# Optimization experiments

Hardware: AMD Instinct MI355X
Metric: run time of the kernel (lower is better)

The kernel has to match this reference:

```python
import jax, jax.numpy as jnp
import numpy as np

D = 1024       # embedding_dim
H = 4096       # mlp_dim
E = 64         # num_experts
K = 3          # top-k
B, S = 2, 2048
C = 512


def setup_inputs() -> dict:
    key = jax.random.key(0)
    ks = jax.random.split(key, 6)
    s = 0.02
    return {
        "x": jax.random.normal(ks[0], (B, S, D), jnp.float32),
        "gate_w": jax.random.normal(ks[1], (D, E), jnp.float32) * s,
        "gate_b": jnp.zeros((E,), jnp.float32),
        "w1": jax.random.normal(ks[2], (E, D, H), jnp.float32) * s,
        "b1": jnp.zeros((E, H), jnp.float32),
        "w2": jax.random.normal(ks[3], (E, H, D), jnp.float32) * s,
        "b2": jnp.zeros((E, D), jnp.float32),
    }


def reference(x, gate_w, gate_b, w1, b1, w2, b2):
    xf = x.reshape(-1, D)                       # [T, D] flattened tokens
    T = xf.shape[0]
    # --- top-k gating (eval mode: clean logits, no noise) ---
    logits = xf @ gate_w + gate_b               # [T, E]
    top_l, top_i = jax.lax.top_k(logits, K)     # [T, K]
    gates = jax.nn.softmax(top_l, axis=-1)      # softmax over the k selected logits
    # --- token permutation / dispatch (capacity-based, order-preserving) ---
    fe = top_i.reshape(-1)                      # [T*K] expert id per assignment
    fg = gates.reshape(-1)                      # [T*K] gate per assignment
    tok = jnp.repeat(jnp.arange(T), K)          # [T*K] source token id
    oh = jax.nn.one_hot(fe, E, dtype=jnp.int32) # [T*K, E]
    pos = (jnp.cumsum(oh, axis=0) * oh).sum(-1) - 1  # slot within expert buffer
    valid = pos < C                             # capacity mask (C sized so nothing drops in practice)
    # scatter tokens into per-expert buffers; OOB (pos>=C) rows dropped
    buf = jnp.zeros((E, C, D), x.dtype).at[fe, pos].set(xf[tok], mode='drop')
    # --- grouped expert MLP: Linear -> exact GELU -> Linear ---
    h = jax.nn.gelu(jnp.einsum('ecd,edh->ech', buf, w1) + b1[:, None, :], approximate=False)
    y = jnp.einsum('ech,ehd->ecd', h, w2) + b2[:, None, :]  # [E, C, D]
    # --- gather back, gate, scatter-add combine ---
    rows = y[fe, jnp.minimum(pos, C - 1)] * (fg * valid.astype(x.dtype))[:, None]
    out = jnp.zeros_like(xf).at[tok].add(rows)
    return out.reshape(x.shape)
```

## Files before the change

kernel.cpp:

```cpp
#include <hip/hip_runtime.h>

#define TTOK 4096
#define DDIM 1024
#define HDIM 4096
#define NEXP 64
#define CAP  512
#define NASN (TTOK*3)

typedef unsigned short u16;
typedef __attribute__((ext_vector_type(8))) short s16x8;
typedef __attribute__((ext_vector_type(4))) short s16x4;
typedef __attribute__((ext_vector_type(4))) float f32x4;

__device__ __forceinline__ u16 f2bf(float f) {
  union { float f; unsigned u; } v; v.f = f;
  unsigned u = v.u;
  return (u16)((u + 0x7fffu + ((u >> 16) & 1u)) >> 16);
}

__device__ __forceinline__ void gl_lds16(const void* g, void* l) {
  __builtin_amdgcn_global_load_lds(
      (const __attribute__((address_space(1))) void*)g,
      (__attribute__((address_space(3))) void*)l, 16, 0, 0);
}

__global__ __launch_bounds__(256) void zero_out(float4* __restrict__ p, int n4) {
  int i = blockIdx.x * 256 + threadIdx.x;
  int st = gridDim.x * 256;
  for (; i < n4; i += st) p[i] = (float4){0.f, 0.f, 0.f, 0.f};
}

__global__ __launch_bounds__(512) void gate_topk(
    const float* __restrict__ x, const float* __restrict__ gw,
    const float* __restrict__ gb, int* __restrict__ fe, float* __restrict__ fg)
{
  int lane = threadIdx.x & 63;
  int wid  = threadIdx.x >> 6;
  int t = blockIdx.x * 8 + wid;
  const float* xr = x + (size_t)t * DDIM;
  float acc = gb[lane];
  #pragma unroll 4
  for (int d = 0; d < DDIM; d++) acc += xr[d] * gw[d * NEXP + lane];

  float v = acc;
  float bv[3]; int bi[3];
  #pragma unroll
  for (int j = 0; j < 3; j++) {
    float mv = v; int mi = lane;
    #pragma unroll
    for (int off = 32; off; off >>= 1) {
      float ov = __shfl_xor(mv, off);
      int   oi = __shfl_xor(mi, off);
      if (ov > mv || (ov == mv && oi < mi)) { mv = ov; mi = oi; }
    }
    bv[j] = mv; bi[j] = mi;
    if (lane == mi) v = -3.4e38f;
  }
  if (lane == 0) {
    float e1 = expf(bv[1] - bv[0]), e2 = expf(bv[2] - bv[0]);
    float inv = 1.0f / (1.0f + e1 + e2);
    fe[t*3+0] = bi[0]; fe[t*3+1] = bi[1]; fe[t*3+2] = bi[2];
    fg[t*3+0] = inv;   fg[t*3+1] = e1*inv; fg[t*3+2] = e2*inv;
  }
}

__global__ __launch_bounds__(64) void scan_pos(
    const int* __restrict__ fe, int* __restrict__ posA,
    int* __restrict__ s2a, int* __restrict__ cnt)
{
  int e = blockIdx.x, lane = threadIdx.x;
  int base = 0;
  for (int i0 = 0; i0 < NASN; i0 += 64) {
    int i = i0 + lane;
    bool m = (fe[i] == e);
    unsigned long long bal = __ballot(m);
    int below = __popcll(bal & ((1ull << lane) - 1ull));
    if (m) {
      int p = base + below;
      posA[i] = p;
      if (p < CAP) s2a[e * CAP + p] = i;
    }
    base += __popcll(bal);
  }
  if (lane == 0) cnt[e] = base < CAP ? base : CAP;
}

__global__ __launch_bounds__(64) void dispatch(
    const float* __restrict__ x, const int* __restrict__ fe,
    const int* __restrict__ posA, u16* __restrict__ bufA)
{
  int a = blockIdx.x;
  int p = posA[a];
  if (p >= CAP) return;
  int e = fe[a];
  int tok = a / 3;
  int l = threadIdx.x;
  const float4* xr = (const float4*)(x + (size_t)tok * DDIM);
  u16* dst = bufA + ((size_t)e * CAP + p) * DDIM;
  #pragma unroll
  for (int j = 0; j < 4; j++) {
    float4 v = xr[j * 64 + l];
    uint2 u;
    u.x = (unsigned)f2bf(v.x) | ((unsigned)f2bf(v.y) << 16);
    u.y = (unsigned)f2bf(v.z) | ((unsigned)f2bf(v.w) << 16);
    *(uint2*)(dst + (size_t)(j * 64 + l) * 4) = u;
  }
}

template<int KTOT, int NTOT, int EPI>
__global__ __launch_bounds__(256, 2) void moe_gemm(
    const u16* __restrict__ Abuf, const float* __restrict__ W,
    const float* __restrict__ bias, u16* __restrict__ hout,
    float* __restrict__ out, const int* __restrict__ cnt,
    const int* __restrict__ s2a, const float* __restrict__ fg, int g0)
{
  constexpr int NCT = NTOT / 128;
  constexpr int NT  = KTOT / 64;
  int NB = gridDim.x;
  int b = blockIdx.x;
  int L = (b & 7) * (NB >> 3) + (b >> 3);
  int tcol = L % NCT;
  int rt   = (L / NCT) & 1;
  int el   = L / (NCT * 2);
  int e    = g0 + el;
  int cnte = cnt[e];
  int c0   = rt * 256;
  if (c0 >= cnte) return;
  int n0 = tcol * 128;

  int tid = threadIdx.x, l = tid & 63, w = tid >> 6;

  __shared__ char AsB[256 * 128];
  __shared__ char BsB[128 * 136];

  const u16* Arows = Abuf + ((size_t)((EPI == 1 ? e : el)) * CAP + c0) * (size_t)KTOT;
  const float* We = W + (size_t)e * KTOT * NTOT;

  int bn = tid & 127, bkg = tid >> 7;
  const float* Wt = We + (size_t)(bkg * 32) * NTOT + n0 + bn;
  char* BsW = BsB + bn * 136 + bkg * 64;

  float brB[32];
  #define LOADB(t) { \
    const float* p_ = Wt + (size_t)(t) * 64 * NTOT; \
    _Pragma("unroll") \
    for (int j_ = 0; j_ < 8; j_++) { \
      _Pragma("unroll") \
      for (int r_ = 0; r_ < 4; r_++) \
        brB[j_ * 4 + r_] = p_[(size_t)(j_ * 4 + r_) * NTOT]; \
    } }
  #define STOREB() { \
    _Pragma("unroll") \
    for (int j_ = 0; j_ < 8; j_++) { \
      uint2 u_; \
      u_.x = (unsigned)f2bf(brB[j_*4+0]) | ((unsigned)f2bf(brB[j_*4+1]) << 16); \
      u_.y = (unsigned)f2bf(brB[j_*4+2]) | ((unsigned)f2bf(brB[j_*4+3]) << 16); \
      *(uint2*)(BsW + j_ * 8) = u_; \
    } }

  f32x4 acc[4][8];
  #pragma unroll
  for (int m = 0; m < 4; m++)
    #pragma unroll
    for (int nn = 0; nn < 8; nn++)
      acc[m][nn] = (f32x4){0.f, 0.f, 0.f, 0.f};

  LOADB(0);

  for (int t = 0; t < NT; ++t) {
    #pragma unroll
    for (int i = 0; i < 8; i++) {
      int r = i * 32 + w * 8 + (l >> 3);
      int cswz = (l & 7) ^ (r & 7);
      const char* gsrc = (const char*)(Arows + (size_t)r * KTOT + (size_t)t * 64) + cswz * 16;
      gl_lds16(gsrc, AsB + (i * 32 + w * 8) * 128);
    }
    STOREB();
    __builtin_amdgcn_sched_barrier(0);
    if (t + 1 < NT) {
      LOADB(t + 1);
      __builtin_amdgcn_sched_barrier(0);
      asm volatile("s_waitcnt vmcnt(32)" ::: "memory");
    } else {
      asm volatile("s_waitcnt vmcnt(0)" ::: "memory");
    }
    asm volatile("s_waitcnt lgkmcnt(0)" ::: "memory");
    __builtin_amdgcn_sched_barrier(0);
    __builtin_amdgcn_s_barrier();
    __builtin_amdgcn_sched_barrier(0);

    #pragma unroll
    for (int k2 = 0; k2 < 2; k2++) {
      int kb = k2 * 32;
      s16x8 af[4], bf8[8];
      #pragma unroll
      for (int m = 0; m < 4; m++) {
        int R = w * 64 + m * 16 + (l & 15);
        int chunk = (kb >> 3) + (l >> 4);
        int sc = chunk ^ (R & 7);
        af[m] = *(const s16x8*)(AsB + R * 128 + sc * 16);
      }
      #pragma unroll
      for (int nn = 0; nn < 8; nn++) {
        int Nn = nn * 16 + (l & 15);
        int kk = kb + (l >> 4) * 8;
        const char* bp = BsB + Nn * 136 + kk * 2;
        union { s16x8 v8; s16x4 v4[2]; } bu;
        bu.v4[0] = *(const s16x4*)bp;
        bu.v4[1] = *(const s16x4*)(bp + 8);
        bf8[nn] = bu.v8;
      }
      #pragma unroll
      for (int m = 0; m < 4; m++)
        #pragma unroll
        for (int nn = 0; nn < 8; nn++)
          acc[m][nn] = __builtin_amdgcn_mfma_f32_16x16x32_bf16(af[m], bf8[nn], acc[m][nn], 0, 0, 0);
    }
    __builtin_amdgcn_s_barrier();
    __builtin_amdgcn_sched_barrier(0);
  }

  int lr = l >> 4, lc = l & 15;
  float bv[8];
  #pragma unroll
  for (int nn = 0; nn < 8; nn++) bv[nn] = bias[(size_t)e * NTOT + n0 + nn * 16 + lc];

  if (EPI == 1) {
    #pragma unroll
    for (int m = 0; m < 4; m++)
      #pragma unroll
      for (int q = 0; q < 4; q++) {
        int rowL = w * 64 + m * 16 + lr * 4 + q;
        if (c0 + rowL < cnte) {
          #pragma unroll
          for (int nn = 0; nn < 8; nn++) {
            float vv = acc[m][nn][q] + bv[nn];
            vv = 0.5f * vv * (1.0f + erff(vv * 0.70710678118f));
            hout[(size_t)(el * CAP + c0 + rowL) * NTOT + (n0 + nn * 16 + lc)] = f2bf(vv);
          }
        }
      }
  } else {
    #pragma unroll
    for (int m = 0; m < 4; m++) {
      int rowbase = w * 64 + m * 16 + lr * 4;
      #pragma unroll
      for (int q = 0; q < 4; q++) {
        int slot = c0 + rowbase + q;
        if (slot < cnte) {
          int aidx = s2a[e * CAP + slot];
          int tok = aidx / 3;
          float gg = fg[aidx];
          #pragma unroll
          for (int nn = 0; nn < 8; nn++) {
            float vv = (acc[m][nn][q] + bv[nn]) * gg;
            atomicAdd(out + (size_t)tok * DDIM + (n0 + nn * 16 + lc), vv);
          }
        }
      }
    }
  }
}

extern "C" void kernel_launch(void* const* d_in, const int* in_sizes, int n_in,
                              void* d_out, int out_size, void* d_ws, size_t ws_size,
                              hipStream_t stream) {
  (void)in_sizes; (void)n_in; (void)ws_size;
  const float* x  = (const float*)d_in[0];
  const float* gw = (const float*)d_in[1];
  const float* gb = (const float*)d_in[2];
  const float* w1 = (const float*)d_in[3];
  const float* b1 = (const float*)d_in[4];
  const float* w2 = (const float*)d_in[5];
  const float* b2 = (const float*)d_in[6];
  float* out = (float*)d_out;

  char* ws = (char*)d_ws;
  int*   fe   = (int*)(ws);
  float* fg   = (float*)(ws + 49152);
  int*   posA = (int*)(ws + 98304);
  int*   s2a  = (int*)(ws + 147456);
  int*   cnt  = (int*)(ws + 278528);
  u16*   bufA = (u16*)(ws + (1 << 20));
  u16*   hbuf = (u16*)(ws + (1 << 20) + 67108864ull);

  zero_out<<<1024, 256, 0, stream>>>((float4*)out, out_size / 4);
  gate_topk<<<TTOK / 8, 512, 0, stream>>>(x, gw, gb, fe, fg);
  scan_pos<<<NEXP, 64, 0, stream>>>(fe, posA, s2a, cnt);
  dispatch<<<NASN, 64, 0, stream>>>(x, fe, posA, bufA);

  moe_gemm<DDIM, HDIM, 1><<<NEXP * 2 * (HDIM / 128), 256, 0, stream>>>(
      bufA, w1, b1, hbuf, nullptr, cnt, nullptr, nullptr, 0);
  moe_gemm<HDIM, DDIM, 2><<<NEXP * 2 * (DDIM / 128), 256, 0, stream>>>(
      hbuf, w2, b2, nullptr, out, cnt, s2a, fg, 0);
}
```

Measured before the change: 742.4 us.

## Use 512-thread blocks and split-K for the down-projection GEMM

Doubles the GEMM block size to 8 waves, so each wave computes 32 rows instead of 64. This halves per-thread accumulator and staging registers and allows higher occupancy via launch bounds (512,4). The second GEMM additionally splits K in two, doubling its grid so more blocks cover the few active tiles. Partial sums are merged through the existing atomicAdd epilogue, with bias added only by the first split. The costs are more atomic traffic, and more waves contending for the same LDS tile with less MFMA work per wave.

```diff
diff --git a/kernel.cpp b/kernel.cpp
--- a/kernel.cpp
+++ b/kernel.cpp
@@ -107,60 +107,61 @@
   }
 }
 
-template<int KTOT, int NTOT, int EPI>
-__global__ __launch_bounds__(256, 2) void moe_gemm(
+template<int KTOT, int NTOT, int EPI, int SK>
+__global__ __launch_bounds__(512, 4) void moe_gemm(
     const u16* __restrict__ Abuf, const float* __restrict__ W,
     const float* __restrict__ bias, u16* __restrict__ hout,
     float* __restrict__ out, const int* __restrict__ cnt,
     const int* __restrict__ s2a, const float* __restrict__ fg, int g0)
 {
   constexpr int NCT = NTOT / 128;
-  constexpr int NT  = KTOT / 64;
+  constexpr int NT  = KTOT / 64 / SK;
   int NB = gridDim.x;
   int b = blockIdx.x;
   int L = (b & 7) * (NB >> 3) + (b >> 3);
   int tcol = L % NCT;
   int rt   = (L / NCT) & 1;
-  int el   = L / (NCT * 2);
+  int rest = L / (NCT * 2);
+  int ks   = rest % SK;
+  int el   = rest / SK;
   int e    = g0 + el;
   int cnte = cnt[e];
   int c0   = rt * 256;
   if (c0 >= cnte) return;
   int n0 = tcol * 128;
+  int koff = ks * (KTOT / SK);
 
   int tid = threadIdx.x, l = tid & 63, w = tid >> 6;
 
   __shared__ char AsB[256 * 128];
   __shared__ char BsB[128 * 136];
 
-  const u16* Arows = Abuf + ((size_t)((EPI == 1 ? e : el)) * CAP + c0) * (size_t)KTOT;
+  const u16* Arows = Abuf + ((size_t)((EPI == 1 ? e : el)) * CAP + c0) * (size_t)KTOT + koff;
   const float* We = W + (size_t)e * KTOT * NTOT;
 
   int bn = tid & 127, bkg = tid >> 7;
-  const float* Wt = We + (size_t)(bkg * 32) * NTOT + n0 + bn;
-  char* BsW = BsB + bn * 136 + bkg * 64;
-
-  float brB[32];
+  const float* Wt = We + (size_t)(koff + bkg * 16) * NTOT + n0 + bn;
+  char* BsW = BsB + bn * 136 + bkg * 32;
+
+  float brB[16];
   #define LOADB(t) { \
     const float* p_ = Wt + (size_t)(t) * 64 * NTOT; \
     _Pragma("unroll") \
-    for (int j_ = 0; j_ < 8; j_++) { \
-      _Pragma("unroll") \
-      for (int r_ = 0; r_ < 4; r_++) \
-        brB[j_ * 4 + r_] = p_[(size_t)(j_ * 4 + r_) * NTOT]; \
-    } }
+    for (int j_ = 0; j_ < 16; j_++) \
+      brB[j_] = p_[(size_t)j_ * NTOT]; \
+    }
   #define STOREB() { \
     _Pragma("unroll") \
-    for (int j_ = 0; j_ < 8; j_++) { \
+    for (int j_ = 0; j_ < 4; j_++) { \
       uint2 u_; \
       u_.x = (unsigned)f2bf(brB[j_*4+0]) | ((unsigned)f2bf(brB[j_*4+1]) << 16); \
       u_.y = (unsigned)f2bf(brB[j_*4+2]) | ((unsigned)f2bf(brB[j_*4+3]) << 16); \
       *(uint2*)(BsW + j_ * 8) = u_; \
     } }
 
-  f32x4 acc[4][8];
-  #pragma unroll
-  for (int m = 0; m < 4; m++)
+  f32x4 acc[2][8];
+  #pragma unroll
+  for (int m = 0; m < 2; m++)
     #pragma unroll
     for (int nn = 0; nn < 8; nn++)
       acc[m][nn] = (f32x4){0.f, 0.f, 0.f, 0.f};
@@ -169,18 +170,18 @@
 
   for (int t = 0; t < NT; ++t) {
     #pragma unroll
-    for (int i = 0; i < 8; i++) {
-      int r = i * 32 + w * 8 + (l >> 3);
+    for (int i = 0; i < 4; i++) {
+      int r = i * 64 + w * 8 + (l >> 3);
       int cswz = (l & 7) ^ (r & 7);
       const char* gsrc = (const char*)(Arows + (size_t)r * KTOT + (size_t)t * 64) + cswz * 16;
-      gl_lds16(gsrc, AsB + (i * 32 + w * 8) * 128);
+      gl_lds16(gsrc, AsB + (i * 64 + w * 8) * 128);
     }
     STOREB();
     __builtin_amdgcn_sched_barrier(0);
     if (t + 1 < NT) {
       LOADB(t + 1);
       __builtin_amdgcn_sched_barrier(0);
-      asm volatile("s_waitcnt vmcnt(32)" ::: "memory");
+      asm volatile("s_waitcnt vmcnt(16)" ::: "memory");
     } else {
       asm volatile("s_waitcnt vmcnt(0)" ::: "memory");
     }
@@ -192,10 +193,10 @@
     #pragma unroll
     for (int k2 = 0; k2 < 2; k2++) {
       int kb = k2 * 32;
-      s16x8 af[4], bf8[8];
-      #pragma unroll
-      for (int m = 0; m < 4; m++) {
-        int R = w * 64 + m * 16 + (l & 15);
+      s16x8 af[2];
+      #pragma unroll
+      for (int m = 0; m < 2; m++) {
+        int R = w * 32 + m * 16 + (l & 15);
         int chunk = (kb >> 3) + (l >> 4);
         int sc = chunk ^ (R & 7);
         af[m] = *(const s16x8*)(AsB + R * 128 + sc * 16);
@@ -208,13 +209,10 @@
         union { s16x8 v8; s16x4 v4[2]; } bu;
         bu.v4[0] = *(const s16x4*)bp;
         bu.v4[1] = *(const s16x4*)(bp + 8);
-        bf8[nn] = bu.v8;
-      }
-      #pragma unroll
-      for (int m = 0; m < 4; m++)
         #pragma unroll
-        for (int nn = 0; nn < 8; nn++)
-          acc[m][nn] = __builtin_amdgcn_mfma_f32_16x16x32_bf16(af[m], bf8[nn], acc[m][nn], 0, 0, 0);
+        for (int m = 0; m < 2; m++)
+          acc[m][nn] = __builtin_amdgcn_mfma_f32_16x16x32_bf16(af[m], bu.v8, acc[m][nn], 0, 0, 0);
+      }
     }
     __builtin_amdgcn_s_barrier();
     __builtin_amdgcn_sched_barrier(0);
@@ -223,14 +221,15 @@
   int lr = l >> 4, lc = l & 15;
   float bv[8];
   #pragma unroll
-  for (int nn = 0; nn < 8; nn++) bv[nn] = bias[(size_t)e * NTOT + n0 + nn * 16 + lc];
+  for (int nn = 0; nn < 8; nn++)
+    bv[nn] = (SK > 1 && ks != 0) ? 0.f : bias[(size_t)e * NTOT + n0 + nn * 16 + lc];
 
   if (EPI == 1) {
     #pragma unroll
-    for (int m = 0; m < 4; m++)
+    for (int m = 0; m < 2; m++)
       #pragma unroll
       for (int q = 0; q < 4; q++) {
-        int rowL = w * 64 + m * 16 + lr * 4 + q;
+        int rowL = w * 32 + m * 16 + lr * 4 + q;
         if (c0 + rowL < cnte) {
           #pragma unroll
           for (int nn = 0; nn < 8; nn++) {
@@ -242,8 +241,8 @@
       }
   } else {
     #pragma unroll
-    for (int m = 0; m < 4; m++) {
-      int rowbase = w * 64 + m * 16 + lr * 4;
+    for (int m = 0; m < 2; m++) {
+      int rowbase = w * 32 + m * 16 + lr * 4;
       #pragma unroll
       for (int q = 0; q < 4; q++) {
         int slot = c0 + rowbase + q;
@@ -289,8 +288,8 @@
   scan_pos<<<NEXP, 64, 0, stream>>>(fe, posA, s2a, cnt);
   dispatch<<<NASN, 64, 0, stream>>>(x, fe, posA, bufA);
 
-  moe_gemm<DDIM, HDIM, 1><<<NEXP * 2 * (HDIM / 128), 256, 0, stream>>>(
+  moe_gemm<DDIM, HDIM, 1, 1><<<NEXP * 2 * (HDIM / 128), 512, 0, stream>>>(
       bufA, w1, b1, hbuf, nullptr, cnt, nullptr, nullptr, 0);
-  moe_gemm<HDIM, DDIM, 2><<<NEXP * 2 * (DDIM / 128), 256, 0, stream>>>(
+  moe_gemm<HDIM, DDIM, 2, 2><<<NEXP * 2 * (DDIM / 128) * 2, 512, 0, stream>>>(
       hbuf, w2, b2, nullptr, out, cnt, s2a, fg, 0);
 }
```

Measured after the change: 793.8 us. +6.9%, slower.
